# Kernel tuning notes

Hardware: AMD Instinct MI355X
Metric: run time of the kernel (lower is better)

Reference implementation:

```python
import jax, jax.numpy as jnp
import numpy as np

N = 131072
F_DIM = 128
HID = 256
POL = 512
EPS = 1e-5


def _lin(key, fan_in, fan_out):
    k1, k2 = jax.random.split(key)
    s = 1.0 / np.sqrt(fan_in)
    W = jax.random.uniform(k1, (fan_in, fan_out), jnp.float32, -s, s)
    b = jax.random.uniform(k2, (fan_out,), jnp.float32, -s, s)
    return W, b


def setup_inputs() -> dict:
    key = jax.random.key(0)
    ks = jax.random.split(key, 12)
    observation = jax.random.normal(ks[0], (N, F_DIM), jnp.float32)
    mask = jnp.ones((N, 1), jnp.float32)
    # dense_to_sparse(eye(N)) -> pure self-loop edge list
    ar = jnp.arange(N, dtype=jnp.int32)
    edge_index = jnp.stack([ar, ar])  # [2, N]
    W1, b1 = _lin(ks[1], F_DIM, HID)
    Wg, bg = _lin(ks[2], HID, HID)     # GCNConv weight/bias
    ln_w = jnp.ones((HID,), jnp.float32)
    ln_b = jnp.zeros((HID,), jnp.float32)
    Wgate, bgate = _lin(ks[3], HID, 1)
    Wd, bd = _lin(ks[4], HID, HID)
    Wp1, bp1 = _lin(ks[5], HID, POL)
    Wp2, bp2 = _lin(ks[6], POL, POL)
    Wv, bv = _lin(ks[7], POL, 1)
    return dict(observation=observation, mask=mask, edge_index=edge_index,
                W1=W1, b1=b1, Wg=Wg, bg=bg, ln_w=ln_w, ln_b=ln_b,
                Wgate=Wgate, bgate=bgate, Wd=Wd, bd=bd,
                Wp1=Wp1, bp1=bp1, Wp2=Wp2, bp2=bp2, Wv=Wv, bv=bv)


def reference(observation, mask, edge_index, W1, b1, Wg, bg, ln_w, ln_b,
              Wgate, bgate, Wd, bd, Wp1, bp1, Wp2, bp2, Wv, bv):
    n = observation.shape[0]
    # encoder_1 + relu
    X = jax.nn.relu(observation @ W1 + b1)  # [N,256]

    # GCNConv(256,256): add self-loops, symmetric norm, gather/scatter
    ar = jnp.arange(n, dtype=edge_index.dtype)
    ei = jnp.concatenate([edge_index, jnp.stack([ar, ar])], axis=1)  # [2,E+N]
    row, col = ei[0], ei[1]
    Xw = X @ Wg
    deg = jax.ops.segment_sum(jnp.ones(ei.shape[1], X.dtype), col, num_segments=n)
    dinv = jnp.where(deg > 0, jax.lax.rsqrt(deg), 0.0)
    norm = dinv[row] * dinv[col]
    msg = Xw[row] * norm[:, None]
    Xg = jax.ops.segment_sum(msg, col, num_segments=n) + bg
    Xg = jax.nn.relu(Xg)

    # PyG LayerNorm, mode='graph' (batch=None): global mean/std over all elements
    mu = Xg.mean()
    sd = jnp.sqrt(jnp.mean((Xg - mu) ** 2))  # std, unbiased=False
    Xn = (Xg - mu) / (sd + EPS) * ln_w + ln_b

    # AttentionalAggregation with sigmoid gate -> [1,256]
    gate = jax.nn.sigmoid(Xn @ Wgate + bgate)  # [N,1]
    pooled = jnp.sum(gate * Xn, axis=0, keepdims=True)

    h = jax.nn.relu(pooled @ Wd + bd)
    h = jax.nn.relu(h @ Wp1 + bp1)
    h = jax.nn.relu(h @ Wp2 + bp2)
    value = h @ Wv + bv  # [1,1]
    return value * mask  # broadcast -> [N,1]
```

## Files before the change

kernel.cpp:

```cpp
#include <hip/hip_runtime.h>

#define NROWS 131072
#define EPSV 1e-5f

typedef __attribute__((ext_vector_type(8))) short short8;
typedef __attribute__((ext_vector_type(4))) short bfx4;
typedef __attribute__((ext_vector_type(4))) float floatx4;

__device__ __forceinline__ short f2bf(float f){
  unsigned u = __builtin_bit_cast(unsigned, f);
  return (short)((u + 0x8000u) >> 16);
}
__device__ __forceinline__ float bf2f(unsigned h){
  unsigned u = h << 16;
  return __builtin_bit_cast(float, u);
}

__device__ __forceinline__ int XIDX(int row, int col){
  return row*256 + ((((col >> 3) ^ (row & 31))) << 3) + (col & 7);
}

__global__ __launch_bounds__(256) void prep_kernel(
    const float* __restrict__ W1, const float* __restrict__ Wg,
    const float* __restrict__ lnw, const float* __restrict__ lnb,
    const float* __restrict__ Wgate,
    short* __restrict__ W1s, short* __restrict__ Wgs,
    float* __restrict__ u, float* accum)
{
  const int b = blockIdx.x, tid = threadIdx.x;
  if (b < 16){
    int idx = b*256 + tid;
    int lane = idx & 63, rg = idx >> 6;
    int ctg = rg & 15, kt = rg >> 4;
    int kb = kt*32 + (lane>>4)*8;
    int c  = ctg*16 + (lane&15);
    short8 t;
    #pragma unroll
    for (int j=0;j<8;j++) t[j] = f2bf(W1[(kb+j)*256 + c]);
    *(short8*)(W1s + idx*8) = t;
  } else if (b < 48){
    int idx = (b-16)*256 + tid;
    int lane = idx & 63, rg = idx >> 6;
    int ctg = rg & 15, kt = rg >> 4;
    int kb = kt*32 + (lane>>4)*8;
    int c  = ctg*16 + (lane&15);
    short8 t;
    #pragma unroll
    for (int j=0;j<8;j++) t[j] = f2bf(Wg[(kb+j)*256 + c]);
    *(short8*)(Wgs + idx*8) = t;
  } else {
    __shared__ float red[8];
    float uv = lnw[tid] * Wgate[tid];
    float lv = lnb[tid] * Wgate[tid];
    u[tid] = uv;
    float a = uv, c = lv;
    #pragma unroll
    for (int off=32; off; off >>= 1){
      a += __shfl_down(a, off);
      c += __shfl_down(c, off);
    }
    const int w = tid >> 6, l = tid & 63;
    if (l == 0){ red[w] = a; red[4+w] = c; }
    __syncthreads();
    if (tid == 0){
      accum[4] = red[0]+red[1]+red[2]+red[3];
      accum[5] = red[4]+red[5]+red[6]+red[7];
    }
  }
}

__global__ __launch_bounds__(256, 3) void gemm12_kernel(
    const float* __restrict__ obs, const float* __restrict__ b1,
    const float* __restrict__ bg,
    const short* __restrict__ W1s, const short* __restrict__ Wgs,
    const float* __restrict__ u,
    short* __restrict__ XgT, float* __restrict__ d, float* __restrict__ pS)
{
  __shared__ short Xs[64*256];
  float* dacc = (float*)Xs;
  short* As = Xs;
  const int tid = threadIdx.x;
  const int w = tid >> 6, l = tid & 63, q = l >> 4, lm = l & 15;
  const long R = (long)blockIdx.x * 64;

  short8 bc[4], bn[4];
  float bias1[4];
  #pragma unroll
  for (int ct=0; ct<4; ct++){
    bc[ct] = *(const short8*)(W1s + (((w*4+ct))*64 + l)*8);
    bias1[ct] = b1[w*64 + ct*16 + lm];
  }

  #pragma unroll
  for (int rt=0; rt<4; rt++){
    const float* ap = obs + (R + rt*16 + lm)*128 + w*32 + q*8;
    floatx4 f0 = *(const floatx4*)ap;
    floatx4 f1 = *(const floatx4*)(ap + 4);
    short8 t;
    t[0]=f2bf(f0[0]); t[1]=f2bf(f0[1]); t[2]=f2bf(f0[2]); t[3]=f2bf(f0[3]);
    t[4]=f2bf(f1[0]); t[5]=f2bf(f1[1]); t[6]=f2bf(f1[2]); t[7]=f2bf(f1[3]);
    *(short8*)(As + ((w*4 + rt)*64 + l)*8) = t;
  }
  __syncthreads();

  floatx4 acc[4][4];
  #pragma unroll
  for (int ct=0; ct<4; ct++){
    floatx4 bi = {bias1[ct], bias1[ct], bias1[ct], bias1[ct]};
    #pragma unroll
    for (int rt=0; rt<4; rt++) acc[rt][ct] = bi;
  }

  short8 ac[4], an[4];
  #pragma unroll
  for (int rt=0; rt<4; rt++)
    ac[rt] = *(const short8*)(As + ((0*4 + rt)*64 + l)*8);
  #pragma unroll
  for (int kt=0; kt<4; kt++){
    if (kt < 3){
      #pragma unroll
      for (int ct=0; ct<4; ct++)
        bn[ct] = *(const short8*)(W1s + (((kt+1)*16 + (w*4+ct))*64 + l)*8);
      #pragma unroll
      for (int rt=0; rt<4; rt++)
        an[rt] = *(const short8*)(As + (((kt+1)*4 + rt)*64 + l)*8);
    }
    #pragma unroll
    for (int ct=0; ct<4; ct++)
      #pragma unroll
      for (int rt=0; rt<4; rt++)
        acc[rt][ct] = __builtin_amdgcn_mfma_f32_16x16x32_bf16(ac[rt], bc[ct], acc[rt][ct], 0,0,0);
    if (kt < 3){
      #pragma unroll
      for (int i=0;i<4;i++){ bc[i]=bn[i]; ac[i]=an[i]; }
    }
  }

  float bias2[4], uc[4];
  #pragma unroll
  for (int ct=0; ct<4; ct++){
    bc[ct] = *(const short8*)(Wgs + (((w*4+ct))*64 + l)*8);
    bias2[ct] = bg[w*64 + ct*16 + lm];
    uc[ct]    = u [w*64 + ct*16 + lm];
  }

  __syncthreads();

  #pragma unroll
  for (int ct=0; ct<4; ct++){
    const int col = w*64 + ct*16 + lm;
    #pragma unroll
    for (int rt=0; rt<4; rt++)
      #pragma unroll
      for (int r=0;r<4;r++)
        Xs[XIDX(rt*16 + q*4 + r, col)] = f2bf(fmaxf(acc[rt][ct][r], 0.f));
  }
  __syncthreads();

  #pragma unroll
  for (int ct=0; ct<4; ct++){
    floatx4 bi = {bias2[ct], bias2[ct], bias2[ct], bias2[ct]};
    #pragma unroll
    for (int rt=0; rt<4; rt++) acc[rt][ct] = bi;
  }
  #pragma unroll
  for (int rt=0; rt<4; rt++)
    ac[rt] = *(const short8*)(Xs + XIDX(rt*16 + lm, 0*32 + q*8));
  #pragma unroll
  for (int kt=0; kt<8; kt++){
    if (kt < 7){
      #pragma unroll
      for (int ct=0; ct<4; ct++)
        bn[ct] = *(const short8*)(Wgs + (((kt+1)*16 + (w*4+ct))*64 + l)*8);
      #pragma unroll
      for (int rt=0; rt<4; rt++)
        an[rt] = *(const short8*)(Xs + XIDX(rt*16 + lm, (kt+1)*32 + q*8));
    }
    #pragma unroll
    for (int ct=0; ct<4; ct++)
      #pragma unroll
      for (int rt=0; rt<4; rt++)
        acc[rt][ct] = __builtin_amdgcn_mfma_f32_16x16x32_bf16(ac[rt], bc[ct], acc[rt][ct], 0,0,0);
    if (kt < 7){
      #pragma unroll
      for (int i=0;i<4;i++){ bc[i]=bn[i]; ac[i]=an[i]; }
    }
  }
  __syncthreads();

  float s1 = 0.f, s2 = 0.f;
  float dp[16];
  #pragma unroll
  for (int i=0;i<16;i++) dp[i] = 0.f;
  #pragma unroll
  for (int ct=0; ct<4; ct++){
    const int col = w*64 + ct*16 + lm;
    const float uv = uc[ct];
    #pragma unroll
    for (int rt=0; rt<4; rt++){
      float v0 = fmaxf(acc[rt][ct][0], 0.f);
      float v1 = fmaxf(acc[rt][ct][1], 0.f);
      float v2 = fmaxf(acc[rt][ct][2], 0.f);
      float v3 = fmaxf(acc[rt][ct][3], 0.f);
      s1 += (v0+v1)+(v2+v3);
      s2 += v0*v0 + v1*v1 + v2*v2 + v3*v3;
      dp[rt*4+0] += v0*uv; dp[rt*4+1] += v1*uv;
      dp[rt*4+2] += v2*uv; dp[rt*4+3] += v3*uv;
      bfx4 pk = {f2bf(v0), f2bf(v1), f2bf(v2), f2bf(v3)};
      *(bfx4*)(XgT + (long)col*NROWS + R + rt*16 + q*4) = pk;
    }
  }
  #pragma unroll
  for (int rt=0; rt<4; rt++)
    #pragma unroll
    for (int r=0; r<4; r++)
      dacc[(w*64 + rt*16 + q*4 + r)*17 + lm] = dp[rt*4+r];

  #pragma unroll
  for (int off=32; off; off >>= 1){
    s1 += __shfl_down(s1, off);
    s2 += __shfl_down(s2, off);
  }
  if (l == 0){
    pS[blockIdx.x*4 + w] = s1;
    pS[8192 + blockIdx.x*4 + w] = s2;
  }
  __syncthreads();

  {
    const int row = tid >> 2, g = tid & 3;
    float s = 0.f;
    #pragma unroll
    for (int wv=0; wv<4; wv++)
      #pragma unroll
      for (int j=0; j<4; j++)
        s += dacc[(wv*64 + row)*17 + g*4 + j];
    s += __shfl_xor(s, 1);
    s += __shfl_xor(s, 2);
    if (g == 0) d[R + row] = s;
  }
}

__global__ __launch_bounds__(256) void pool_kernel(
    const short* __restrict__ XgT, const float* __restrict__ dvec,
    const float* __restrict__ bgate, const float* __restrict__ pS,
    const float* __restrict__ accum,
    float* __restrict__ gxPart, float* __restrict__ gsPart)
{
  __shared__ float red[8];
  __shared__ float spj[4][8];
  __shared__ float sgs[4];
  const int tid = threadIdx.x, w = tid >> 6, l = tid & 63;

  float a = 0.f, b = 0.f;
  #pragma unroll
  for (int i=0;i<32;i++){
    a += pS[tid + 256*i];
    b += pS[8192 + tid + 256*i];
  }
  #pragma unroll
  for (int off=32; off; off >>= 1){
    a += __shfl_down(a, off);
    b += __shfl_down(b, off);
  }
  if (l == 0){ red[w] = a; red[4+w] = b; }
  __syncthreads();
  const float NE = (float)NROWS * 256.f;
  const float S1 = red[0]+red[1]+red[2]+red[3];
  const float S2 = red[4]+red[5]+red[6]+red[7];
  const float mu = S1 / NE;
  float var = S2 / NE - mu*mu;
  var = var > 0.f ? var : 0.f;
  const float inv = 1.f / (sqrtf(var) + EPSV);
  const float gc = -inv*mu*accum[4] + accum[5] + bgate[0];

  const int rs = blockIdx.x >> 5, cg = blockIdx.x & 31, c0 = cg*8;
  float p[8];
  #pragma unroll
  for (int j=0;j<8;j++) p[j] = 0.f;
  float gs = 0.f;

  #pragma unroll
  for (int it=0; it<4; it++){
    const int r0 = rs*4096 + it*1024 + tid*4;
    floatx4 dv = *(const floatx4*)(dvec + r0);
    float g0 = 1.f/(1.f + __expf(-(inv*dv[0] + gc)));
    float g1 = 1.f/(1.f + __expf(-(inv*dv[1] + gc)));
    float g2 = 1.f/(1.f + __expf(-(inv*dv[2] + gc)));
    float g3 = 1.f/(1.f + __expf(-(inv*dv[3] + gc)));
    gs += (g0+g1)+(g2+g3);
    #pragma unroll
    for (int j=0;j<8;j++){
      bfx4 xv = *(const bfx4*)(XgT + (long)(c0+j)*NROWS + r0);
      p[j] += g0*bf2f((unsigned short)xv[0]) + g1*bf2f((unsigned short)xv[1])
            + g2*bf2f((unsigned short)xv[2]) + g3*bf2f((unsigned short)xv[3]);
    }
  }
  #pragma unroll
  for (int j=0;j<8;j++)
    #pragma unroll
    for (int off=32; off; off >>= 1) p[j] += __shfl_down(p[j], off);
  #pragma unroll
  for (int off=32; off; off >>= 1) gs += __shfl_down(gs, off);
  if (l == 0){
    #pragma unroll
    for (int j=0;j<8;j++) spj[w][j] = p[j];
    sgs[w] = gs;
  }
  __syncthreads();
  if (tid < 8)
    gxPart[rs*256 + c0 + tid] = spj[0][tid]+spj[1][tid]+spj[2][tid]+spj[3][tid];
  if (cg == 0 && tid == 8)
    gsPart[rs] = sgs[0]+sgs[1]+sgs[2]+sgs[3];
}

__global__ __launch_bounds__(256) void mlp1_kernel(
    const float* __restrict__ lnw, const float* __restrict__ lnb,
    const float* __restrict__ Wd,  const float* __restrict__ bd,
    const float* __restrict__ pS,  const float* __restrict__ gxPart,
    const float* __restrict__ gsPart, float* __restrict__ h1)
{
  __shared__ float xa[256];
  __shared__ float red[9];
  __shared__ float sp[4][64];
  const int tid = threadIdx.x, w = tid >> 6, l = tid & 63;

  {
    float a = 0.f, b = 0.f;
    #pragma unroll
    for (int i=0;i<32;i++){
      a += pS[tid + 256*i];
      b += pS[8192 + tid + 256*i];
    }
    #pragma unroll
    for (int off=32; off; off >>= 1){
      a += __shfl_down(a, off);
      b += __shfl_down(b, off);
    }
    if (l == 0){ red[w] = a; red[4+w] = b; }
  }
  if (w == 0){
    float gg = (l < 32) ? gsPart[l] : 0.f;
    #pragma unroll
    for (int off=32; off; off >>= 1) gg += __shfl_down(gg, off);
    if (l == 0) red[8] = gg;
  }
  __syncthreads();
  const float NE = (float)NROWS * 256.f;
  const float mu = (red[0]+red[1]+red[2]+red[3]) / NE;
  float var = (red[4]+red[5]+red[6]+red[7]) / NE - mu*mu;
  var = var > 0.f ? var : 0.f;
  const float inv = 1.f / (sqrtf(var) + EPSV);
  const float G = red[8];

  {
    float sgx = 0.f;
    #pragma unroll
    for (int s=0;s<32;s++) sgx += gxPart[s*256 + tid];
    const float lw = lnw[tid];
    xa[tid] = inv*lw*sgx + (lnb[tid] - mu*inv*lw)*G;
  }
  __syncthreads();

  const int j = blockIdx.x*64 + l;
  const int k0 = w*64;
  const float* wp = Wd + (long)k0*256 + j;
  float p0=0.f,p1=0.f,p2=0.f,p3=0.f;
  #pragma unroll
  for (int k=0; k<64; k+=4){
    p0 += xa[k0+k  ] * wp[(k  )*256];
    p1 += xa[k0+k+1] * wp[(k+1)*256];
    p2 += xa[k0+k+2] * wp[(k+2)*256];
    p3 += xa[k0+k+3] * wp[(k+3)*256];
  }
  sp[w][l] = (p0+p1)+(p2+p3);
  __syncthreads();
  if (w == 0)
    h1[j] = fmaxf(sp[0][l]+sp[1][l]+sp[2][l]+sp[3][l] + bd[j], 0.f);
}

__global__ __launch_bounds__(256) void mlp_mid(
    const float* __restrict__ W, const float* __restrict__ bias,
    const float* __restrict__ x, float* __restrict__ y,
    const int inDim, const int outDim)
{
  __shared__ float sp[4][64];
  const int l = threadIdx.x & 63, w = threadIdx.x >> 6;
  const int j = blockIdx.x*64 + l;
  const int kq = inDim >> 2, k0 = w*kq;
  const float* wp = W + (long)k0*outDim + j;
  float p0=0.f,p1=0.f,p2=0.f,p3=0.f;
  for (int k=0; k<kq; k+=4){
    p0 += x[k0+k  ] * wp[(long)(k  )*outDim];
    p1 += x[k0+k+1] * wp[(long)(k+1)*outDim];
    p2 += x[k0+k+2] * wp[(long)(k+2)*outDim];
    p3 += x[k0+k+3] * wp[(long)(k+3)*outDim];
  }
  sp[w][l] = (p0+p1)+(p2+p3);
  __syncthreads();
  if (w == 0)
    y[j] = fmaxf(sp[0][l]+sp[1][l]+sp[2][l]+sp[3][l] + bias[j], 0.f);
}

__global__ __launch_bounds__(256) void bcast_kernel(
    const float* __restrict__ h3, const float* __restrict__ Wv,
    const float* __restrict__ bv, const float* __restrict__ mask,
    float* __restrict__ out)
{
  __shared__ float red[4];
  const int tid = threadIdx.x, w = tid >> 6, l = tid & 63;
  float p = h3[tid]*Wv[tid] + h3[tid+256]*Wv[tid+256];
  #pragma unroll
  for (int off=32; off; off >>= 1) p += __shfl_down(p, off);
  if (l == 0) red[w] = p;
  __syncthreads();
  const float value = red[0]+red[1]+red[2]+red[3] + bv[0];

  const long i = (long)blockIdx.x*256 + tid;
  floatx4 m = *(const floatx4*)(mask + i*4);
  floatx4 o = {m[0]*value, m[1]*value, m[2]*value, m[3]*value};
  *(floatx4*)(out + i*4) = o;
}

extern "C" void kernel_launch(void* const* d_in, const int* in_sizes, int n_in,
                              void* d_out, int out_size, void* d_ws, size_t ws_size,
                              hipStream_t stream)
{
  const float* obs   = (const float*)d_in[0];
  const float* mask  = (const float*)d_in[1];
  const float* W1    = (const float*)d_in[3];
  const float* b1    = (const float*)d_in[4];
  const float* Wg    = (const float*)d_in[5];
  const float* bg    = (const float*)d_in[6];
  const float* lnw   = (const float*)d_in[7];
  const float* lnb   = (const float*)d_in[8];
  const float* Wgate = (const float*)d_in[9];
  const float* bgate = (const float*)d_in[10];
  const float* Wd    = (const float*)d_in[11];
  const float* bd    = (const float*)d_in[12];
  const float* Wp1   = (const float*)d_in[13];
  const float* bp1   = (const float*)d_in[14];
  const float* Wp2   = (const float*)d_in[15];
  const float* bp2   = (const float*)d_in[16];
  const float* Wv    = (const float*)d_in[17];
  const float* bv    = (const float*)d_in[18];
  float* out = (float*)d_out;

  char* wsb = (char*)d_ws;
  short* XgT   = (short*)(wsb);
  short* W1s   = (short*)(wsb + 67108864);
  short* Wgs   = (short*)(wsb + 67174400);
  float* u     = (float*)(wsb + 67305472);
  float* dvec  = (float*)(wsb + 67306496);
  float* pS    = (float*)(wsb + 67830784);
  float* gxP   = (float*)(wsb + 67896320);
  float* gsP   = (float*)(wsb + 67929088);
  float* accum = (float*)(wsb + 67930112);
  float* h1    = (float*)(wsb + 67931136);
  float* h2    = (float*)(wsb + 67932160);
  float* h3    = (float*)(wsb + 67934208);

  prep_kernel<<<49, 256, 0, stream>>>(W1, Wg, lnw, lnb, Wgate, W1s, Wgs, u, accum);
  gemm12_kernel<<<2048, 256, 0, stream>>>(obs, b1, bg, W1s, Wgs, u, XgT, dvec, pS);
  pool_kernel<<<1024, 256, 0, stream>>>(XgT, dvec, bgate, pS, accum, gxP, gsP);
  mlp1_kernel<<<4, 256, 0, stream>>>(lnw, lnb, Wd, bd, pS, gxP, gsP, h1);
  mlp_mid<<<8, 256, 0, stream>>>(Wp1, bp1, h1, h2, 256, 512);
  mlp_mid<<<8, 256, 0, stream>>>(Wp2, bp2, h2, h3, 512, 512);
  bcast_kernel<<<128, 256, 0, stream>>>(h3, Wv, bv, mask, out);
}
```

Baseline: 216.6 us.

## Make gemm12 persistent over four row tiles with prefetched observation loads

The fused two-GEMM kernel now has each block process four consecutive 64-row tiles in a loop, launching 512 blocks instead of 2048. The next tile's fp32 observation rows are loaded into registers while the current tile's MFMAs run, to hide global load latency. The per-block statistics partials are reduced in shared memory to one value per block, so the downstream pool and mlp1 kernels read far fewer partials. The cost is more registers for the prefetch buffers and fewer blocks, which could lower occupancy and leave the 256 CUs less evenly loaded.

```diff
diff --git a/kernel.cpp b/kernel.cpp
--- a/kernel.cpp
+++ b/kernel.cpp
@@ -77,167 +77,191 @@
     short* __restrict__ XgT, float* __restrict__ d, float* __restrict__ pS)
 {
   __shared__ short Xs[64*256];
+  __shared__ float red2[8];
   float* dacc = (float*)Xs;
   short* As = Xs;
   const int tid = threadIdx.x;
   const int w = tid >> 6, l = tid & 63, q = l >> 4, lm = l & 15;
-  const long R = (long)blockIdx.x * 64;
-
-  short8 bc[4], bn[4];
-  float bias1[4];
+  const long RB = (long)blockIdx.x * 256;
+
+  float bias1[4], bias2[4], uc[4];
   #pragma unroll
   for (int ct=0; ct<4; ct++){
-    bc[ct] = *(const short8*)(W1s + (((w*4+ct))*64 + l)*8);
     bias1[ct] = b1[w*64 + ct*16 + lm];
-  }
-
-  #pragma unroll
-  for (int rt=0; rt<4; rt++){
-    const float* ap = obs + (R + rt*16 + lm)*128 + w*32 + q*8;
-    floatx4 f0 = *(const floatx4*)ap;
-    floatx4 f1 = *(const floatx4*)(ap + 4);
-    short8 t;
-    t[0]=f2bf(f0[0]); t[1]=f2bf(f0[1]); t[2]=f2bf(f0[2]); t[3]=f2bf(f0[3]);
-    t[4]=f2bf(f1[0]); t[5]=f2bf(f1[1]); t[6]=f2bf(f1[2]); t[7]=f2bf(f1[3]);
-    *(short8*)(As + ((w*4 + rt)*64 + l)*8) = t;
-  }
-  __syncthreads();
-
-  floatx4 acc[4][4];
-  #pragma unroll
-  for (int ct=0; ct<4; ct++){
-    floatx4 bi = {bias1[ct], bias1[ct], bias1[ct], bias1[ct]};
-    #pragma unroll
-    for (int rt=0; rt<4; rt++) acc[rt][ct] = bi;
-  }
-
-  short8 ac[4], an[4];
-  #pragma unroll
-  for (int rt=0; rt<4; rt++)
-    ac[rt] = *(const short8*)(As + ((0*4 + rt)*64 + l)*8);
-  #pragma unroll
-  for (int kt=0; kt<4; kt++){
-    if (kt < 3){
-      #pragma unroll
-      for (int ct=0; ct<4; ct++)
-        bn[ct] = *(const short8*)(W1s + (((kt+1)*16 + (w*4+ct))*64 + l)*8);
-      #pragma unroll
-      for (int rt=0; rt<4; rt++)
-        an[rt] = *(const short8*)(As + (((kt+1)*4 + rt)*64 + l)*8);
-    }
-    #pragma unroll
-    for (int ct=0; ct<4; ct++)
-      #pragma unroll
-      for (int rt=0; rt<4; rt++)
-        acc[rt][ct] = __builtin_amdgcn_mfma_f32_16x16x32_bf16(ac[rt], bc[ct], acc[rt][ct], 0,0,0);
-    if (kt < 3){
-      #pragma unroll
-      for (int i=0;i<4;i++){ bc[i]=bn[i]; ac[i]=an[i]; }
-    }
-  }
-
-  float bias2[4], uc[4];
-  #pragma unroll
-  for (int ct=0; ct<4; ct++){
-    bc[ct] = *(const short8*)(Wgs + (((w*4+ct))*64 + l)*8);
     bias2[ct] = bg[w*64 + ct*16 + lm];
     uc[ct]    = u [w*64 + ct*16 + lm];
   }
 
-  __syncthreads();
-
-  #pragma unroll
-  for (int ct=0; ct<4; ct++){
-    const int col = w*64 + ct*16 + lm;
+  floatx4 pf[4][2];
+  #pragma unroll
+  for (int rt=0; rt<4; rt++){
+    const float* ap = obs + (RB + rt*16 + lm)*128 + w*32 + q*8;
+    pf[rt][0] = *(const floatx4*)ap;
+    pf[rt][1] = *(const floatx4*)(ap + 4);
+  }
+
+  float s1 = 0.f, s2 = 0.f;
+
+  for (int t=0; t<4; ++t){
+    const long R = RB + t*64;
+
+    short8 bc[4], bn[4], ac[4], an[4];
+    #pragma unroll
+    for (int ct=0; ct<4; ct++)
+      bc[ct] = *(const short8*)(W1s + ((w*4+ct)*64 + l)*8);
+    #pragma unroll
+    for (int rt=0; rt<4; rt++){
+      short8 tt;
+      tt[0]=f2bf(pf[rt][0][0]); tt[1]=f2bf(pf[rt][0][1]);
+      tt[2]=f2bf(pf[rt][0][2]); tt[3]=f2bf(pf[rt][0][3]);
+      tt[4]=f2bf(pf[rt][1][0]); tt[5]=f2bf(pf[rt][1][1]);
+      tt[6]=f2bf(pf[rt][1][2]); tt[7]=f2bf(pf[rt][1][3]);
+      *(short8*)(As + ((w*4 + rt)*64 + l)*8) = tt;
+    }
+    __syncthreads();
+
+    if (t < 3){
+      #pragma unroll
+      for (int rt=0; rt<4; rt++){
+        const float* ap = obs + (R + 64 + rt*16 + lm)*128 + w*32 + q*8;
+        pf[rt][0] = *(const floatx4*)ap;
+        pf[rt][1] = *(const floatx4*)(ap + 4);
+      }
+    }
+
+    floatx4 acc[4][4];
+    #pragma unroll
+    for (int ct=0; ct<4; ct++){
+      floatx4 bi = {bias1[ct], bias1[ct], bias1[ct], bias1[ct]};
+      #pragma unroll
+      for (int rt=0; rt<4; rt++) acc[rt][ct] = bi;
+    }
+
     #pragma unroll
     for (int rt=0; rt<4; rt++)
-      #pragma unroll
-      for (int r=0;r<4;r++)
-        Xs[XIDX(rt*16 + q*4 + r, col)] = f2bf(fmaxf(acc[rt][ct][r], 0.f));
-  }
-  __syncthreads();
-
-  #pragma unroll
-  for (int ct=0; ct<4; ct++){
-    floatx4 bi = {bias2[ct], bias2[ct], bias2[ct], bias2[ct]};
-    #pragma unroll
-    for (int rt=0; rt<4; rt++) acc[rt][ct] = bi;
-  }
-  #pragma unroll
-  for (int rt=0; rt<4; rt++)
-    ac[rt] = *(const short8*)(Xs + XIDX(rt*16 + lm, 0*32 + q*8));
-  #pragma unroll
-  for (int kt=0; kt<8; kt++){
-    if (kt < 7){
+      ac[rt] = *(const short8*)(As + ((0*4 + rt)*64 + l)*8);
+    #pragma unroll
+    for (int kt=0; kt<4; kt++){
+      if (kt < 3){
+        #pragma unroll
+        for (int ct=0; ct<4; ct++)
+          bn[ct] = *(const short8*)(W1s + (((kt+1)*16 + (w*4+ct))*64 + l)*8);
+        #pragma unroll
+        for (int rt=0; rt<4; rt++)
+          an[rt] = *(const short8*)(As + (((kt+1)*4 + rt)*64 + l)*8);
+      }
       #pragma unroll
       for (int ct=0; ct<4; ct++)
-        bn[ct] = *(const short8*)(Wgs + (((kt+1)*16 + (w*4+ct))*64 + l)*8);
+        #pragma unroll
+        for (int rt=0; rt<4; rt++)
+          acc[rt][ct] = __builtin_amdgcn_mfma_f32_16x16x32_bf16(ac[rt], bc[ct], acc[rt][ct], 0,0,0);
+      if (kt < 3){
+        #pragma unroll
+        for (int i=0;i<4;i++){ bc[i]=bn[i]; ac[i]=an[i]; }
+      }
+    }
+
+    #pragma unroll
+    for (int ct=0; ct<4; ct++)
+      bc[ct] = *(const short8*)(Wgs + (((w*4+ct))*64 + l)*8);
+
+    __syncthreads();
+
+    #pragma unroll
+    for (int ct=0; ct<4; ct++){
+      const int col = w*64 + ct*16 + lm;
       #pragma unroll
       for (int rt=0; rt<4; rt++)
-        an[rt] = *(const short8*)(Xs + XIDX(rt*16 + lm, (kt+1)*32 + q*8));
-    }
-    #pragma unroll
-    for (int ct=0; ct<4; ct++)
-      #pragma unroll
-      for (int rt=0; rt<4; rt++)
-        acc[rt][ct] = __builtin_amdgcn_mfma_f32_16x16x32_bf16(ac[rt], bc[ct], acc[rt][ct], 0,0,0);
-    if (kt < 7){
-      #pragma unroll
-      for (int i=0;i<4;i++){ bc[i]=bn[i]; ac[i]=an[i]; }
-    }
-  }
-  __syncthreads();
-
-  float s1 = 0.f, s2 = 0.f;
-  float dp[16];
-  #pragma unroll
-  for (int i=0;i<16;i++) dp[i] = 0.f;
-  #pragma unroll
-  for (int ct=0; ct<4; ct++){
-    const int col = w*64 + ct*16 + lm;
-    const float uv = uc[ct];
-    #pragma unroll
-    for (int rt=0; rt<4; rt++){
-      float v0 = fmaxf(acc[rt][ct][0], 0.f);
-      float v1 = fmaxf(acc[rt][ct][1], 0.f);
-      float v2 = fmaxf(acc[rt][ct][2], 0.f);
-      float v3 = fmaxf(acc[rt][ct][3], 0.f);
-      s1 += (v0+v1)+(v2+v3);
-      s2 += v0*v0 + v1*v1 + v2*v2 + v3*v3;
-      dp[rt*4+0] += v0*uv; dp[rt*4+1] += v1*uv;
-      dp[rt*4+2] += v2*uv; dp[rt*4+3] += v3*uv;
-      bfx4 pk = {f2bf(v0), f2bf(v1), f2bf(v2), f2bf(v3)};
-      *(bfx4*)(XgT + (long)col*NROWS + R + rt*16 + q*4) = pk;
-    }
-  }
-  #pragma unroll
-  for (int rt=0; rt<4; rt++)
-    #pragma unroll
-    for (int r=0; r<4; r++)
-      dacc[(w*64 + rt*16 + q*4 + r)*17 + lm] = dp[rt*4+r];
+        #pragma unroll
+        for (int r=0;r<4;r++)
+          Xs[XIDX(rt*16 + q*4 + r, col)] = f2bf(fmaxf(acc[rt][ct][r], 0.f));
+    }
+    __syncthreads();
+
+    #pragma unroll
+    for (int ct=0; ct<4; ct++){
+      floatx4 bi = {bias2[ct], bias2[ct], bias2[ct], bias2[ct]};
+      #pragma unroll
+      for (int rt=0; rt<4; rt++) acc[rt][ct] = bi;
+    }
+    #pragma unroll
+    for (int rt=0; rt<4; rt++)
+      ac[rt] = *(const short8*)(Xs + XIDX(rt*16 + lm, 0*32 + q*8));
+    #pragma unroll
+    for (int kt=0; kt<8; kt++){
+      if (kt < 7){
+        #pragma unroll
+        for (int ct=0; ct<4; ct++)
+          bn[ct] = *(const short8*)(Wgs + (((kt+1)*16 + (w*4+ct))*64 + l)*8);
+        #pragma unroll
+        for (int rt=0; rt<4; rt++)
+          an[rt] = *(const short8*)(Xs + XIDX(rt*16 + lm, (kt+1)*32 + q*8));
+      }
+      #pragma unroll
+      for (int ct=0; ct<4; ct++)
+        #pragma unroll
+        for (int rt=0; rt<4; rt++)
+          acc[rt][ct] = __builtin_amdgcn_mfma_f32_16x16x32_bf16(ac[rt], bc[ct], acc[rt][ct], 0,0,0);
+      if (kt < 7){
+        #pragma unroll
+        for (int i=0;i<4;i++){ bc[i]=bn[i]; ac[i]=an[i]; }
+      }
+    }
+    __syncthreads();
+
+    float dp[16];
+    #pragma unroll
+    for (int i=0;i<16;i++) dp[i] = 0.f;
+    #pragma unroll
+    for (int ct=0; ct<4; ct++){
+      const int col = w*64 + ct*16 + lm;
+      const float uv = uc[ct];
+      #pragma unroll
+      for (int rt=0; rt<4; rt++){
+        float v0 = fmaxf(acc[rt][ct][0], 0.f);
+        float v1 = fmaxf(acc[rt][ct][1], 0.f);
+        float v2 = fmaxf(acc[rt][ct][2], 0.f);
+        float v3 = fmaxf(acc[rt][ct][3], 0.f);
+        s1 += (v0+v1)+(v2+v3);
+        s2 += v0*v0 + v1*v1 + v2*v2 + v3*v3;
+        dp[rt*4+0] += v0*uv; dp[rt*4+1] += v1*uv;
+        dp[rt*4+2] += v2*uv; dp[rt*4+3] += v3*uv;
+        bfx4 pk = {f2bf(v0), f2bf(v1), f2bf(v2), f2bf(v3)};
+        *(bfx4*)(XgT + (long)col*NROWS + R + rt*16 + q*4) = pk;
+      }
+    }
+    #pragma unroll
+    for (int rt=0; rt<4; rt++)
+      #pragma unroll
+      for (int r=0; r<4; r++)
+        dacc[(w*64 + rt*16 + q*4 + r)*17 + lm] = dp[rt*4+r];
+    __syncthreads();
+
+    {
+      const int row = tid >> 2, g = tid & 3;
+      float s = 0.f;
+      #pragma unroll
+      for (int wv=0; wv<4; wv++)
+        #pragma unroll
+        for (int j=0; j<4; j++)
+          s += dacc[(wv*64 + row)*17 + g*4 + j];
+      s += __shfl_xor(s, 1);
+      s += __shfl_xor(s, 2);
+      if (g == 0) d[R + row] = s;
+    }
+    __syncthreads();
+  }
 
   #pragma unroll
   for (int off=32; off; off >>= 1){
     s1 += __shfl_down(s1, off);
     s2 += __shfl_down(s2, off);
   }
-  if (l == 0){
-    pS[blockIdx.x*4 + w] = s1;
-    pS[8192 + blockIdx.x*4 + w] = s2;
-  }
-  __syncthreads();
-
-  {
-    const int row = tid >> 2, g = tid & 3;
-    float s = 0.f;
-    #pragma unroll
-    for (int wv=0; wv<4; wv++)
-      #pragma unroll
-      for (int j=0; j<4; j++)
-        s += dacc[(wv*64 + row)*17 + g*4 + j];
-    s += __shfl_xor(s, 1);
-    s += __shfl_xor(s, 2);
-    if (g == 0) d[R + row] = s;
+  if (l == 0){ red2[w] = s1; red2[4+w] = s2; }
+  __syncthreads();
+  if (tid == 0){
+    pS[blockIdx.x]       = red2[0]+red2[1]+red2[2]+red2[3];
+    pS[512 + blockIdx.x] = red2[4]+red2[5]+red2[6]+red2[7];
   }
 }
 
@@ -252,12 +276,8 @@
   __shared__ float sgs[4];
   const int tid = threadIdx.x, w = tid >> 6, l = tid & 63;
 
-  float a = 0.f, b = 0.f;
-  #pragma unroll
-  for (int i=0;i<32;i++){
-    a += pS[tid + 256*i];
-    b += pS[8192 + tid + 256*i];
-  }
+  float a = pS[tid]       + pS[tid + 256];
+  float b = pS[512 + tid] + pS[768 + tid];
   #pragma unroll
   for (int off=32; off; off >>= 1){
     a += __shfl_down(a, off);
@@ -326,12 +346,8 @@
   const int tid = threadIdx.x, w = tid >> 6, l = tid & 63;
 
   {
-    float a = 0.f, b = 0.f;
-    #pragma unroll
-    for (int i=0;i<32;i++){
-      a += pS[tid + 256*i];
-      b += pS[8192 + tid + 256*i];
-    }
+    float a = pS[tid]       + pS[tid + 256];
+    float b = pS[512 + tid] + pS[768 + tid];
     #pragma unroll
     for (int off=32; off; off >>= 1){
       a += __shfl_down(a, off);
@@ -461,7 +477,7 @@
   float* h3    = (float*)(wsb + 67934208);
 
   prep_kernel<<<49, 256, 0, stream>>>(W1, Wg, lnw, lnb, Wgate, W1s, Wgs, u, accum);
-  gemm12_kernel<<<2048, 256, 0, stream>>>(obs, b1, bg, W1s, Wgs, u, XgT, dvec, pS);
+  gemm12_kernel<<<512, 256, 0, stream>>>(obs, b1, bg, W1s, Wgs, u, XgT, dvec, pS);
   pool_kernel<<<1024, 256, 0, stream>>>(XgT, dvec, bgate, pS, accum, gxP, gsP);
   mlp1_kernel<<<4, 256, 0, stream>>>(lnw, lnb, Wd, bd, pS, gxP, gsP, h1);
   mlp_mid<<<8, 256, 0, stream>>>(Wp1, bp1, h1, h2, 256, 512);
```

Measured after the change: 363.4 us. 67.7% more time.
